# Kernel tuning notes

Hardware: AMD Instinct MI355X
Metric: run time of the kernel (lower is better)

The kernel has to match this reference:

```python
import jax, jax.numpy as jnp
import numpy as np

LN_EPS = 1e-5  # torch LayerNorm default
EPS = 1e-8     # slot-attention eps

def _ln(x, g, b):
    m = jnp.mean(x, axis=-1, keepdims=True)
    v = jnp.mean(jnp.square(x - m), axis=-1, keepdims=True)
    return (x - m) * jax.lax.rsqrt(v + LN_EPS) * g + b

def setup_inputs() -> dict:
    key = jax.random.key(0)
    ks = jax.random.split(key, 16)
    b, d, n_s, h = 131072, 256, 16, 256
    w_scale = d ** -0.5
    return {
        "inputs": jax.random.normal(ks[0], (b, 1, d), jnp.float32),
        "noise": jax.random.normal(ks[1], (n_s, d), jnp.float32),
        "slots_mu": jax.random.normal(ks[2], (1, d), jnp.float32),
        "slots_sigma": jax.random.uniform(ks[3], (1, d), jnp.float32),
        "Wq": jax.random.normal(ks[4], (d, d), jnp.float32) * w_scale,
        "bq": jnp.zeros((d,), jnp.float32),
        "Wk": jax.random.normal(ks[5], (d, d), jnp.float32) * w_scale,
        "bk": jnp.zeros((d,), jnp.float32),
        "Wv": jax.random.normal(ks[6], (d, d), jnp.float32) * w_scale,
        "bv": jnp.zeros((d,), jnp.float32),
        "W_ih": jax.random.normal(ks[7], (3 * d, d), jnp.float32) * w_scale,
        "W_hh": jax.random.normal(ks[8], (3 * d, d), jnp.float32) * w_scale,
        "b_ih": jnp.zeros((3 * d,), jnp.float32),
        "b_hh": jnp.zeros((3 * d,), jnp.float32),
        "W1": jax.random.normal(ks[9], (h, d), jnp.float32) * w_scale,
        "b1": jnp.zeros((h,), jnp.float32),
        "W2": jax.random.normal(ks[10], (d, h), jnp.float32) * (h ** -0.5),
        "b2": jnp.zeros((d,), jnp.float32),
        "g_in": jnp.ones((d,), jnp.float32),
        "be_in": jnp.zeros((d,), jnp.float32),
        "g_s": jnp.ones((d,), jnp.float32),
        "be_s": jnp.zeros((d,), jnp.float32),
        "g_f": jnp.ones((d,), jnp.float32),
        "be_f": jnp.zeros((d,), jnp.float32),
    }

def reference(inputs, noise, slots_mu, slots_sigma, Wq, bq, Wk, bk, Wv, bv,
              W_ih, W_hh, b_ih, b_hh, W1, b1, W2, b2,
              g_in, be_in, g_s, be_s, g_f, be_f):
    b, w, d = inputs.shape  # w == 1 required by the module's LayerNorm(dim)
    x = inputs.reshape(b, w * d)
    scale = d ** -0.5
    iters = 3

    slots = slots_mu + slots_sigma * noise  # (n_s, d), reparameterized normal

    x = _ln(x, g_in, be_in)
    k = x @ Wk.T + bk  # (b, d)
    v = x @ Wv.T + bv  # (b, d)

    for _ in range(iters):
        slots_prev = slots
        s = _ln(slots, g_s, be_s)
        q = s @ Wq.T + bq                      # (n_s, d)
        dots = jnp.einsum('nd,bd->nb', q, k) * scale
        attn = jax.nn.softmax(dots, axis=0) + EPS   # softmax over slots
        attn = attn / jnp.sum(attn, axis=-1, keepdims=True)
        updates = jnp.einsum('bd,nb->nd', v, attn)  # (n_s, d)
        # torch GRUCell
        gx = updates @ W_ih.T + b_ih                # (n_s, 3d)
        gh = slots_prev @ W_hh.T + b_hh
        xr, xz, xn = jnp.split(gx, 3, axis=-1)
        hr, hz, hn = jnp.split(gh, 3, axis=-1)
        r = jax.nn.sigmoid(xr + hr)
        z = jax.nn.sigmoid(xz + hz)
        n = jnp.tanh(xn + r * hn)
        slots = (1.0 - z) * n + z * slots_prev
        ff = jax.nn.relu(_ln(slots, g_f, be_f) @ W1.T + b1) @ W2.T + b2
        slots = slots + ff
    return slots
```

## Files before the change

### kernel.cpp

```cpp
#include <hip/hip_runtime.h>
#include <stdint.h>

#define B_ROWS 131072
#define SCALE 0.0625f
#define LN_EPS 1e-5f
#define ATTN_EPS 1e-8f

#define BIG_BLOCKS 512
#define BIG_THREADS 512
#define ROWS_PER_BLOCK (B_ROWS / BIG_BLOCKS)
#define ROWS_PER_WAVE  (ROWS_PER_BLOCK / 8)
#define NSLICE BIG_BLOCKS

#define WS_PARTU 0
#define WS_PARTS (WS_PARTU + NSLICE*4096)
#define WS_U     (WS_PARTS + NSLICE*16)
#define WS_S     (WS_U + 4096)
#define WS_SLOTS (WS_S + 64)
#define WS_MID   (WS_SLOTS + 4096)
#define WS_GX    (WS_MID + 4096)
#define WS_GH    (WS_GX + 12288)
#define WS_H1    (WS_GH + 12288)
#define WS_QKG   (WS_H1 + 4096)
#define WS_QB    (WS_QKG + 4096)
#define WS_WIHV  (WS_QB + 64)
#define WS_BGX   (WS_WIHV + 196608)
#define WS_WQKG  (WS_BGX + 768)
#define WS_U2G   (WS_WQKG + 65536)
#define WS_U1    (WS_U2G + 256)
#define WS_C1    (WS_U1 + 256)

__global__ __launch_bounds__(256) void k_pre1(
    const float* __restrict__ Wq, const float* __restrict__ bq,
    const float* __restrict__ Wk, const float* __restrict__ bk,
    const float* __restrict__ Wv, const float* __restrict__ bv,
    const float* __restrict__ W_ih, const float* __restrict__ b_ih,
    const float* __restrict__ g_in, const float* __restrict__ be_in,
    float* __restrict__ ws)
{
  int bid = blockIdx.x, t = threadIdx.x;
  int wave = t >> 6, lane = t & 63;
  if (bid < 192) {
    __shared__ __align__(16) float sW[4 * 256];
    __shared__ __align__(16) float sBv[256];
    int j0 = bid * 4;
#pragma unroll
    for (int r = 0; r < 4; r++) sW[r * 256 + t] = W_ih[(j0 + r) * 256 + t];
    sBv[t] = bv[t];
    __syncthreads();
    int d = t;
    float a0 = 0.f, a1 = 0.f, a2 = 0.f, a3 = 0.f;
#pragma unroll 8
    for (int dd = 0; dd < 256; dd++) {
      float v = Wv[dd * 256 + d];
      a0 = fmaf(sW[0 * 256 + dd], v, a0);
      a1 = fmaf(sW[1 * 256 + dd], v, a1);
      a2 = fmaf(sW[2 * 256 + dd], v, a2);
      a3 = fmaf(sW[3 * 256 + dd], v, a3);
    }
    ws[WS_WIHV + (j0 + 0) * 256 + d] = a0;
    ws[WS_WIHV + (j0 + 1) * 256 + d] = a1;
    ws[WS_WIHV + (j0 + 2) * 256 + d] = a2;
    ws[WS_WIHV + (j0 + 3) * 256 + d] = a3;
    float s = 0.f;
#pragma unroll
    for (int q = 0; q < 4; q++) {
      int idx = lane * 4 + q;
      s = fmaf(sW[wave * 256 + idx], sBv[idx], s);
    }
#pragma unroll
    for (int m = 1; m <= 32; m <<= 1) s += __shfl_xor(s, m);
    if (lane == 0) ws[WS_BGX + j0 + wave] = b_ih[j0 + wave] + s;
  } else if (bid < 256) {
    __shared__ __align__(16) float sKc[4 * 256];
    __shared__ __align__(16) float sBq[256];
    int c0 = (bid - 192) * 4;
#pragma unroll
    for (int r = 0; r < 4; r++) sKc[r * 256 + t] = Wk[t * 256 + c0 + r];
    sBq[t] = bq[t];
    __syncthreads();
    int d = t;
    float a0 = 0.f, a1 = 0.f, a2 = 0.f, a3 = 0.f;
#pragma unroll 8
    for (int i = 0; i < 256; i++) {
      float wq = Wq[i * 256 + d];
      a0 = fmaf(wq, sKc[0 * 256 + i], a0);
      a1 = fmaf(wq, sKc[1 * 256 + i], a1);
      a2 = fmaf(wq, sKc[2 * 256 + i], a2);
      a3 = fmaf(wq, sKc[3 * 256 + i], a3);
    }
    ws[WS_WQKG + (c0 + 0) * 256 + d] = SCALE * g_in[c0 + 0] * a0;
    ws[WS_WQKG + (c0 + 1) * 256 + d] = SCALE * g_in[c0 + 1] * a1;
    ws[WS_WQKG + (c0 + 2) * 256 + d] = SCALE * g_in[c0 + 2] * a2;
    ws[WS_WQKG + (c0 + 3) * 256 + d] = SCALE * g_in[c0 + 3] * a3;
    float s = 0.f;
#pragma unroll
    for (int q = 0; q < 4; q++) {
      int idx = lane * 4 + q;
      s = fmaf(sBq[idx], sKc[wave * 256 + idx], s);
    }
#pragma unroll
    for (int m = 1; m <= 32; m <<= 1) s += __shfl_xor(s, m);
    if (lane == 0) ws[WS_U2G + c0 + wave] = SCALE * g_in[c0 + wave] * s;
  } else {
    __shared__ __align__(16) float sBe[256];
    __shared__ __align__(16) float sT2[256];
    sBe[t] = be_in[t];
    __syncthreads();
    float a = 0.f;
#pragma unroll 8
    for (int dp = 0; dp < 256; dp += 4) {
      float4 w = *(const float4*)(Wk + t * 256 + dp);
      a = fmaf(w.x, sBe[dp], fmaf(w.y, sBe[dp + 1],
          fmaf(w.z, sBe[dp + 2], fmaf(w.w, sBe[dp + 3], a))));
    }
    sT2[t] = a + bk[t];
    __syncthreads();
    float u = 0.f;
#pragma unroll 8
    for (int i = 0; i < 256; i++)
      u = fmaf(Wq[i * 256 + t], sT2[i], u);
    ws[WS_U1 + t] = u;
    if (wave == 0) {
      float s = 0.f;
// ... 52 lines not shown
    int cr = t >> 6, n = (t >> 2) & 15, ks = t & 3;
    int c = bid * 4 + cr;
    const float* wrow = ws + WS_WQKG + c * 256 + ks * 64;
    const float* srow = &sS[n * 260 + ks * 64];
    float acc = 0.f;
#pragma unroll
    for (int i = 0; i < 16; i++) {
      float4 w = *(const float4*)(wrow + i * 4);
      float4 s4 = *(const float4*)(srow + i * 4);
      acc = fmaf(w.x, s4.x, fmaf(w.y, s4.y, fmaf(w.z, s4.z, fmaf(w.w, s4.w, acc))));
    }
    sAux[t] = acc;
    __syncthreads();
    if (t < 64) {
      int cr2 = t >> 4, n2 = t & 15;
      int c2 = bid * 4 + cr2;
      int b = cr2 * 64 + n2 * 4;
      float s = sAux[b] + sAux[b + 1] + sAux[b + 2] + sAux[b + 3];
      ws[WS_QKG + n2 * 256 + c2] = s + ws[WS_U2G + c2];
    }
  } else {
    int n = t >> 4, ks = t & 15;
    float acc = 0.f;
    for (int k = 0; k < 16; k++)
      acc = fmaf(sS[n * 260 + ks * 16 + k], ws[WS_U1 + ks * 16 + k], acc);
    sAux[t] = acc;
    __syncthreads();
    if (t < 16) {
      float s = 0.f;
      for (int k = 0; k < 16; k++) s += sAux[t * 16 + k];
      ws[WS_QB + t] = SCALE * (s + ws[WS_C1]);
    }
  }
}

__global__ __launch_bounds__(512, 2) void k_big(
    const float* __restrict__ X, float* __restrict__ ws)
{
  __shared__ __align__(16) float red[4 * 4096];
  __shared__ __align__(16) float redS[128];
  int t = threadIdx.x;
  int wave = t >> 6, lane = t & 63;
  int p = lane >> 4, g = lane & 15;

  const float* qkg = ws + WS_QKG;
  float qw[4][16];
  float qs[4];
#pragma unroll
  for (int i = 0; i < 4; i++) {
    const float* rp = qkg + (4 * p + i) * 256 + g * 16;
#pragma unroll
    for (int jq = 0; jq < 4; jq++) {
      float4 v4 = *(const float4*)(rp + 4 * jq);
      qw[i][4 * jq + 0] = v4.x; qw[i][4 * jq + 1] = v4.y;
      qw[i][4 * jq + 2] = v4.z; qw[i][4 * jq + 3] = v4.w;
    }
    float s = 0.f;
#pragma unroll
    for (int j = 0; j < 16; j++) s += qw[i][j];
    qs[i] = s;
  }
#pragma unroll
  for (int m = 1; m <= 8; m <<= 1) {
#pragma unroll
    for (int i = 0; i < 4; i++) qs[i] += __shfl_xor(qs[i], m);
  }
  float qb0[4];
  {
    float4 q4 = *(const float4*)(ws + WS_QB + 4 * p);
    qb0[0] = q4.x; qb0[1] = q4.y; qb0[2] = q4.z; qb0[3] = q4.w;
  }

  float P[4][16];
#pragma unroll
  for (int i = 0; i < 4; i++)
#pragma unroll
    for (int j = 0; j < 16; j++) P[i][j] = 0.f;
  float Q[4] = {0.f, 0.f, 0.f, 0.f};
  float Sa[4] = {0.f, 0.f, 0.f, 0.f};

  size_t rowbase = (size_t)blockIdx.x * ROWS_PER_BLOCK + (size_t)wave * ROWS_PER_WAVE;
  const float* base = X + rowbase * 256 + g * 16;

  float4 cA0 = *(const float4*)(base + 0);
  float4 cB0 = *(const float4*)(base + 4);
  float4 cC0 = *(const float4*)(base + 8);
  float4 cD0 = *(const float4*)(base + 12);
  float4 cA1 = *(const float4*)(base + 256);
  float4 cB1 = *(const float4*)(base + 260);
  float4 cC1 = *(const float4*)(base + 264);
  float4 cD1 = *(const float4*)(base + 268);

#pragma unroll 1
  for (int r = 0; r < ROWS_PER_WAVE; r += 2) {
    const float* nx = base + (size_t)((r + 2 < ROWS_PER_WAVE) ? (r + 2) : 0) * 256;
    float4 pA0 = *(const float4*)(nx + 0);
    float4 pB0 = *(const float4*)(nx + 4);
    float4 pC0 = *(const float4*)(nx + 8);
    float4 pD0 = *(const float4*)(nx + 12);
    float4 pA1 = *(const float4*)(nx + 256);
    float4 pB1 = *(const float4*)(nx + 260);
    float4 pC1 = *(const float4*)(nx + 264);
    float4 pD1 = *(const float4*)(nx + 268);

    float x0[16], x1[16];
    x0[0] = cA0.x; x0[1] = cA0.y; x0[2] = cA0.z; x0[3] = cA0.w;
    x0[4] = cB0.x; x0[5] = cB0.y; x0[6] = cB0.z; x0[7] = cB0.w;
    x0[8] = cC0.x; x0[9] = cC0.y; x0[10] = cC0.z; x0[11] = cC0.w;
    x0[12] = cD0.x; x0[13] = cD0.y; x0[14] = cD0.z; x0[15] = cD0.w;
    x1[0] = cA1.x; x1[1] = cA1.y; x1[2] = cA1.z; x1[3] = cA1.w;
    x1[4] = cB1.x; x1[5] = cB1.y; x1[6] = cB1.z; x1[7] = cB1.w;
    x1[8] = cC1.x; x1[9] = cC1.y; x1[10] = cC1.z; x1[11] = cC1.w;
    x1[12] = cD1.x; x1[13] = cD1.y; x1[14] = cD1.z; x1[15] = cD1.w;

    float s10 = 0.f, s20 = 0.f, s11 = 0.f, s21 = 0.f;
#pragma unroll
    for (int j = 0; j < 16; j++) {
      s10 += x0[j]; s20 = fmaf(x0[j], x0[j], s20);
      s11 += x1[j]; s21 = fmaf(x1[j], x1[j], s21);
    }
#pragma unroll
    for (int m = 1; m <= 8; m <<= 1) {
      s10 += __shfl_xor(s10, m); s11 += __shfl_xor(s11, m);
      s20 += __shfl_xor(s20, m); s21 += __shfl_xor(s21, m);
    }
    float mean0 = s10 * (1.f / 256.f), mean1 = s11 * (1.f / 256.f);
    float var0 = fmaxf(fmaf(-mean0, mean0, s20 * (1.f / 256.f)), 0.f);
    float var1 = fmaxf(fmaf(-mean1, mean1, s21 * (1.f / 256.f)), 0.f);
    float rs0 = rsqrtf(var0 + LN_EPS), rs1 = rsqrtf(var1 + LN_EPS);
    float mrs0 = mean0 * rs0, mrs1 = mean1 * rs1;

    float d0[4] = {0.f, 0.f, 0.f, 0.f};
    float d1[4] = {0.f, 0.f, 0.f, 0.f};
#pragma unroll
    for (int j = 0; j < 16; j++) {
#pragma unroll
      for (int i = 0; i < 4; i++) {
        d0[i] = fmaf(qw[i][j], x0[j], d0[i]);
        d1[i] = fmaf(qw[i][j], x1[j], d1[i]);
      }
    }
#pragma unroll
    for (int m = 1; m <= 8; m <<= 1) {
#pragma unroll
      for (int i = 0; i < 4; i++) {
        d0[i] += __shfl_xor(d0[i], m);
        d1[i] += __shfl_xor(d1[i], m);
      }
    }
    float dsc0[4], dsc1[4];
#pragma unroll
    for (int i = 0; i < 4; i++) {
      dsc0[i] = fmaf(rs0, d0[i], fmaf(-mrs0, qs[i], qb0[i]));
      dsc1[i] = fmaf(rs1, d1[i], fmaf(-mrs1, qs[i], qb0[i]));
    }

    float mx0 = fmaxf(fmaxf(dsc0[0], dsc0[1]), fmaxf(dsc0[2], dsc0[3]));
    float mx1 = fmaxf(fmaxf(dsc1[0], dsc1[1]), fmaxf(dsc1[2], dsc1[3]));
    mx0 = fmaxf(mx0, __shfl_xor(mx0, 16)); mx1 = fmaxf(mx1, __shfl_xor(mx1, 16));
    mx0 = fmaxf(mx0, __shfl_xor(mx0, 32)); mx1 = fmaxf(mx1, __shfl_xor(mx1, 32));
    float e0[4], e1[4];
#pragma unroll
    for (int i = 0; i < 4; i++) {
      e0[i] = __expf(dsc0[i] - mx0);
      e1[i] = __expf(dsc1[i] - mx1);
    }
    float se0 = e0[0] + e0[1] + e0[2] + e0[3];
    float se1 = e1[0] + e1[1] + e1[2] + e1[3];
    se0 += __shfl_xor(se0, 16); se1 += __shfl_xor(se1, 16);
    se0 += __shfl_xor(se0, 32); se1 += __shfl_xor(se1, 32);
    float inv0 = 1.0f / se0, inv1 = 1.0f / se1;
    float a0v[4], ar0[4], a1v[4], ar1[4];
#pragma unroll
    for (int i = 0; i < 4; i++) {
      a0v[i] = fmaf(e0[i], inv0, ATTN_EPS); ar0[i] = a0v[i] * rs0;
      a1v[i] = fmaf(e1[i], inv1, ATTN_EPS); ar1[i] = a1v[i] * rs1;
    }

#pragma unroll
    for (int j = 0; j < 16; j++) {
#pragma unroll
      for (int i = 0; i < 4; i++) {
        P[i][j] = fmaf(ar0[i], x0[j], P[i][j]);
        P[i][j] = fmaf(ar1[i], x1[j], P[i][j]);
      }
    }
#pragma unroll
    for (int i = 0; i < 4; i++) {
      Q[i] = fmaf(a0v[i], mrs0, Q[i]);
      Q[i] = fmaf(a1v[i], mrs1, Q[i]);
      Sa[i] += a0v[i];
      Sa[i] += a1v[i];
    }

    cA0 = pA0; cB0 = pB0; cC0 = pC0; cD0 = pD0;
    cA1 = pA1; cB1 = pB1; cC1 = pC1; cD1 = pD1;
  }

  int slot = wave & 3;
  if (wave < 4) {
#pragma unroll
    for (int i = 0; i < 4; i++) {
#pragma unroll
      for (int jq = 0; jq < 4; jq++) {
        float4 v4;
        v4.x = P[i][4 * jq + 0] - Q[i]; v4.y = P[i][4 * jq + 1] - Q[i];
        v4.z = P[i][4 * jq + 2] - Q[i]; v4.w = P[i][4 * jq + 3] - Q[i];
        *(float4*)&red[slot * 4096 + (4 * p + i) * 256 + g * 16 + jq * 4] = v4;
      }
    }
  }
  if (g == 0) {
#pragma unroll
    for (int i = 0; i < 4; i++) redS[wave * 16 + 4 * p + i] = Sa[i];
  }
  __syncthreads();
  if (wave >= 4) {
#pragma unroll
    for (int i = 0; i < 4; i++) {
#pragma unroll
      for (int jq = 0; jq < 4; jq++) {
        float4* dst = (float4*)&red[slot * 4096 + (4 * p + i) * 256 + g * 16 + jq * 4];
        float4 c = *dst;
        c.x += P[i][4 * jq + 0] - Q[i]; c.y += P[i][4 * jq + 1] - Q[i];
        c.z += P[i][4 * jq + 2] - Q[i]; c.w += P[i][4 * jq + 3] - Q[i];
        *dst = c;
      }
    }
  }
  __syncthreads();
#pragma unroll
  for (int k = 0; k < 8; k++) {
    int idx = k * 512 + t;
    float v = red[idx] + red[4096 + idx] + red[8192 + idx] + red[12288 + idx];
    ws[WS_PARTU + (size_t)blockIdx.x * 4096 + idx] = v;
  }
  if (t < 16) {
    float sv = 0.f;
#pragma unroll
    for (int w = 0; w < 8; w++) sv += redS[w * 16 + t];
    ws[WS_PARTS + blockIdx.x * 16 + t] = sv;
  }
}

__global__ __launch_bounds__(256) void k_red(float* __restrict__ ws)
{
  __shared__ __align__(16) float sAux[256];
  int bid = blockIdx.x, t = threadIdx.x;
  if (bid < 256) {
    int el = t & 15, wg = t >> 4;
    int e = bid * 16 + el;
    float acc = 0.f;
#pragma unroll 8
    for (int k = 0; k < 32; k++)
      acc += ws[WS_PARTU + (size_t)(wg + k * 16) * 4096 + e];
    sAux[t] = acc;
    __syncthreads();
    if (t < 16) {
      float s = 0.f;
      for (int w = 0; w < 16; w++) s += sAux[w * 16 + t];
      ws[WS_U + bid * 16 + t] = s;
    }
  } else {
    int n = t & 15, wg = t >> 4;
    float acc = 0.f;
#pragma unroll 8
    for (int k = 0; k < 32; k++)
      acc += ws[WS_PARTS + (wg + k * 16) * 16 + n];
    sAux[t] = acc;
    __syncthreads();
    if (t < 16) {
      float s = 0.f;
      for (int w = 0; w < 16; w++) s += sAux[w * 16 + t];
      ws[WS_S + t] = s;
    }
  }
}

__global__ __launch_bounds__(256) void k_gxgh(
    const float* __restrict__ W_hh, const float* __restrict__ b_hh,
    const float* __restrict__ g_in, const float* __restrict__ be_in,
    float* __restrict__ ws)
{
  __shared__ __align__(16) float sU[16 * 260];
  __shared__ __align__(16) float sInv[16];
  int bid = blockIdx.x, t = threadIdx.x;
  bool isgx = bid < 64;
  if (isgx && t < 16) sInv[t] = 1.0f / ws[WS_S + t];
  __syncthreads();
  if (isgx) {
    float gi = g_in[t], bi = be_in[t];
    for (int n = 0; n < 16; n++)
      sU[n * 260 + t] = fmaf(gi * ws[WS_U + n * 256 + t], sInv[n], bi);
  } else {
    for (int n = 0; n < 16; n++)
      sU[n * 260 + t] = ws[WS_SLOTS + n * 256 + t];
  }
  __syncthreads();
  int jr = t >> 4, n = t & 15;
  if (jr < 12) {
    int j = (isgx ? bid : bid - 64) * 12 + jr;
    const float* srow = &sU[n * 260];
    const float* wrow = isgx ? (ws + WS_WIHV + j * 256) : (W_hh + j * 256);
    float acc = isgx ? ws[WS_BGX + j] : b_hh[j];
#pragma unroll 8
    for (int k = 0; k < 64; k++) {
      float4 w = *(const float4*)(wrow + k * 4);
      float4 s4 = *(const float4*)(srow + k * 4);
      acc = fmaf(w.x, s4.x, fmaf(w.y, s4.y, fmaf(w.z, s4.z, fmaf(w.w, s4.w, acc))));
    }
    if (isgx) ws[WS_GX + n * 768 + j] = acc;
    else      ws[WS_GH + n * 768 + j] = acc;
  }
}

__global__ __launch_bounds__(256) void k_midh1(
    const float* __restrict__ W1, const float* __restrict__ b1,
    const float* __restrict__ g_f, const float* __restrict__ be_f,
    float* __restrict__ ws)
{
  __shared__ __align__(16) float sM[16 * 260];
  __shared__ __align__(16) float sAux[512];
  __shared__ __align__(16) float sStat[32];
  int bid = blockIdx.x, t = threadIdx.x;
  for (int n = 0; n < 16; n++) {
    float xr = ws[WS_GX + n * 768 + t],       hr = ws[WS_GH + n * 768 + t];
    float xz = ws[WS_GX + n * 768 + 256 + t], hz = ws[WS_GH + n * 768 + 256 + t];
    float xn = ws[WS_GX + n * 768 + 512 + t], hn = ws[WS_GH + n * 768 + 512 + t];
    float sp = ws[WS_SLOTS + n * 256 + t];
    float r = 1.f / (1.f + __expf(-(xr + hr)));
    float z = 1.f / (1.f + __expf(-(xz + hz)));
    float nn = tanhf(fmaf(r, hn, xn));
    float mid = fmaf(z, sp - nn, nn);
    sM[n * 260 + t] = mid;
    if (bid == 0) ws[WS_MID + n * 256 + t] = mid;
  }
  __syncthreads();
  { int n = t >> 4, c = t & 15;
    float s1 = 0.f, s2 = 0.f;
    for (int k = 0; k < 16; k++) {
      float x = sM[n * 260 + c * 16 + k];
      s1 += x; s2 = fmaf(x, x, s2);
    }
    sAux[n * 16 + c] = s1; sAux[256 + n * 16 + c] = s2; }
  __syncthreads();
  if (t < 16) {
    float s1 = 0.f, s2 = 0.f;
    for (int c = 0; c < 16; c++) { s1 += sAux[t * 16 + c]; s2 += sAux[256 + t * 16 + c]; }
    float m = s1 * (1.f / 256.f);
    float v = fmaxf(fmaf(-m, m, s2 * (1.f / 256.f)), 0.f);
    sStat[t] = m; sStat[16 + t] = rsqrtf(v + LN_EPS);
  }
  __syncthreads();
  { float gf = g_f[t], bf = be_f[t];
    for (int n = 0; n < 16; n++) {
      float m = sStat[n], rs = sStat[16 + n];
      sM[n * 260 + t] = fmaf((sM[n * 260 + t] - m) * rs, gf, bf);
    } }
  __syncthreads();
  int jr = t >> 6, n = (t >> 2) & 15, ks = t & 3;
  int j = bid * 4 + jr;
  const float* wrow = W1 + j * 256 + ks * 64;
  const float* srow = &sM[n * 260 + ks * 64];
  float acc = 0.f;
#pragma unroll
  for (int k = 0; k < 16; k++) {
    float4 w = *(const float4*)(wrow + k * 4);
    float4 s4 = *(const float4*)(srow + k * 4);
    acc = fmaf(w.x, s4.x, fmaf(w.y, s4.y, fmaf(w.z, s4.z, fmaf(w.w, s4.w, acc))));
  }
  sAux[t] = acc;
  __syncthreads();
  if (t < 64) {
    int jr2 = t >> 4, n2 = t & 15;
    int j2 = bid * 4 + jr2;
    int b = jr2 * 64 + n2 * 4;
    float s = sAux[b] + sAux[b + 1] + sAux[b + 2] + sAux[b + 3] + b1[j2];
    ws[WS_H1 + n2 * 256 + j2] = fmaxf(s, 0.f);
  }
}

__global__ __launch_bounds__(256) void k_ffnew(
    const float* __restrict__ W2, const float* __restrict__ b2v,
    float* __restrict__ out, float* __restrict__ ws)
{
  __shared__ __align__(16) float sH[16 * 260];
  __shared__ __align__(16) float sAux[256];
  int bid = blockIdx.x, t = threadIdx.x;
  for (int n = 0; n < 16; n++)
    sH[n * 260 + t] = ws[WS_H1 + n * 256 + t];
  __syncthreads();
  int dr = t >> 6, n = (t >> 2) & 15, ks = t & 3;
  int d = bid * 4 + dr;
  const float* wrow = W2 + d * 256 + ks * 64;
  const float* srow = &sH[n * 260 + ks * 64];
  float acc = 0.f;
#pragma unroll
  for (int k = 0; k < 16; k++) {
    float4 w = *(const float4*)(wrow + k * 4);
    float4 s4 = *(const float4*)(srow + k * 4);
    acc = fmaf(w.x, s4.x, fmaf(w.y, s4.y, fmaf(w.z, s4.z, fmaf(w.w, s4.w, acc))));
  }
  sAux[t] = acc;
  __syncthreads();
  if (t < 64) {
    int dr2 = t >> 4, n2 = t & 15;
    int d2 = bid * 4 + dr2;
    int b = dr2 * 64 + n2 * 4;
    float s = sAux[b] + sAux[b + 1] + sAux[b + 2] + sAux[b + 3]
            + b2v[d2] + ws[WS_MID + n2 * 256 + d2];
    ws[WS_SLOTS + n2 * 256 + d2] = s;
    out[n2 * 256 + d2] = s;
  }
}

extern "C" void kernel_launch(void* const* d_in, const int* in_sizes, int n_in,
                              void* d_out, int out_size, void* d_ws, size_t ws_size,
                              hipStream_t stream)
{
  (void)in_sizes; (void)n_in; (void)out_size; (void)ws_size;
  const float* inputs = (const float*)d_in[0];
  const float* noise  = (const float*)d_in[1];
  const float* mu     = (const float*)d_in[2];
  const float* sigma  = (const float*)d_in[3];
  const float* Wq     = (const float*)d_in[4];
  const float* bq     = (const float*)d_in[5];
  const float* Wk     = (const float*)d_in[6];
  const float* bk     = (const float*)d_in[7];
  const float* Wv     = (const float*)d_in[8];
  const float* bv     = (const float*)d_in[9];
  const float* W_ih   = (const float*)d_in[10];
  const float* W_hh   = (const float*)d_in[11];
  const float* b_ih   = (const float*)d_in[12];
  const float* b_hh   = (const float*)d_in[13];
  const float* W1     = (const float*)d_in[14];
  const float* b1     = (const float*)d_in[15];
  const float* W2     = (const float*)d_in[16];
  const float* b2     = (const float*)d_in[17];
  const float* g_in   = (const float*)d_in[18];
  const float* be_in  = (const float*)d_in[19];
  const float* g_s    = (const float*)d_in[20];
  const float* be_s   = (const float*)d_in[21];
  const float* g_f    = (const float*)d_in[22];
  const float* be_f   = (const float*)d_in[23];
  float* ws = (float*)d_ws;
  float* out = (float*)d_out;

  hipLaunchKernelGGL(k_pre1, dim3(257), dim3(256), 0, stream,
                     Wq, bq, Wk, bk, Wv, bv, W_ih, b_ih, g_in, be_in, ws);
  hipLaunchKernelGGL(k_qkg, dim3(65), dim3(256), 0, stream,
                     noise, mu, sigma, g_s, be_s, ws, 1);
  for (int it = 0; it < 3; it++) {
    hipLaunchKernelGGL(k_big, dim3(BIG_BLOCKS), dim3(BIG_THREADS), 0, stream, inputs, ws);
    hipLaunchKernelGGL(k_red, dim3(257), dim3(256), 0, stream, ws);
    hipLaunchKernelGGL(k_gxgh, dim3(128), dim3(256), 0, stream,
                       W_hh, b_hh, g_in, be_in, ws);
    hipLaunchKernelGGL(k_midh1, dim3(64), dim3(256), 0, stream,
                       W1, b1, g_f, be_f, ws);
    hipLaunchKernelGGL(k_ffnew, dim3(64), dim3(256), 0, stream,
                       W2, b2, out, ws);
    if (it < 2)
      hipLaunchKernelGGL(k_qkg, dim3(65), dim3(256), 0, stream,
                         noise, mu, sigma, g_s, be_s, ws, 0);
  }
}
```

Before: 551.0 us.

## Fuse per-iteration slot update chain into one per-slot kernel

Replaces the reduction, GRU gate GEMVs, LayerNorm+MLP and next-iteration query prep kernels with a single kernel that runs one 512-thread block per slot. Each block reduces the partial updates for its slot, computes the GRU, feed-forward and next query/key projection with wave-shuffle dot products, and writes the new slots. This removes four launches and their global round trips per iteration. In exchange only 16 blocks run, and each block rereads all the weight matrices, so the grid is very narrow and leans on cache bandwidth.

```diff
diff --git a/kernel.cpp b/kernel.cpp
--- a/kernel.cpp
+++ b/kernel.cpp
@@ -30,6 +30,28 @@
 #define WS_U1    (WS_U2G + 256)
 #define WS_C1    (WS_U1 + 256)
 
+__device__ __forceinline__ float dot16(const float* __restrict__ w, const float* s)
+{
+  float4 w0 = *(const float4*)(w);
+  float4 w1 = *(const float4*)(w + 4);
+  float4 w2 = *(const float4*)(w + 8);
+  float4 w3 = *(const float4*)(w + 12);
+  float4 s0 = *(const float4*)(s);
+  float4 s1 = *(const float4*)(s + 4);
+  float4 s2 = *(const float4*)(s + 8);
+  float4 s3 = *(const float4*)(s + 12);
+  float a = 0.f;
+  a = fmaf(w0.x, s0.x, a); a = fmaf(w0.y, s0.y, a);
+  a = fmaf(w0.z, s0.z, a); a = fmaf(w0.w, s0.w, a);
+  a = fmaf(w1.x, s1.x, a); a = fmaf(w1.y, s1.y, a);
+  a = fmaf(w1.z, s1.z, a); a = fmaf(w1.w, s1.w, a);
+  a = fmaf(w2.x, s2.x, a); a = fmaf(w2.y, s2.y, a);
+  a = fmaf(w2.z, s2.z, a); a = fmaf(w2.w, s2.w, a);
+  a = fmaf(w3.x, s3.x, a); a = fmaf(w3.y, s3.y, a);
+  a = fmaf(w3.z, s3.z, a); a = fmaf(w3.w, s3.w, a);
+  return a;
+}
+
 __global__ __launch_bounds__(256) void k_pre1(
     const float* __restrict__ Wq, const float* __restrict__ bq,
     const float* __restrict__ Wk, const float* __restrict__ bk,
@@ -419,174 +441,166 @@
   }
 }
 
-__global__ __launch_bounds__(256) void k_red(float* __restrict__ ws)
-{
-  __shared__ __align__(16) float sAux[256];
-  int bid = blockIdx.x, t = threadIdx.x;
-  if (bid < 256) {
-    int el = t & 15, wg = t >> 4;
-    int e = bid * 16 + el;
-    float acc = 0.f;
-#pragma unroll 8
-    for (int k = 0; k < 32; k++)
-      acc += ws[WS_PARTU + (size_t)(wg + k * 16) * 4096 + e];
-    sAux[t] = acc;
-    __syncthreads();
-    if (t < 16) {
-      float s = 0.f;
-      for (int w = 0; w < 16; w++) s += sAux[w * 16 + t];
-      ws[WS_U + bid * 16 + t] = s;
-    }
-  } else {
-    int n = t & 15, wg = t >> 4;
-    float acc = 0.f;
-#pragma unroll 8
-    for (int k = 0; k < 32; k++)
-      acc += ws[WS_PARTS + (wg + k * 16) * 16 + n];
-    sAux[t] = acc;
-    __syncthreads();
-    if (t < 16) {
-      float s = 0.f;
-      for (int w = 0; w < 16; w++) s += sAux[w * 16 + t];
-      ws[WS_S + t] = s;
-    }
-  }
-}
-
-__global__ __launch_bounds__(256) void k_gxgh(
+__global__ __launch_bounds__(512) void k_slot2(
     const float* __restrict__ W_hh, const float* __restrict__ b_hh,
     const float* __restrict__ g_in, const float* __restrict__ be_in,
-    float* __restrict__ ws)
-{
-  __shared__ __align__(16) float sU[16 * 260];
-  __shared__ __align__(16) float sInv[16];
-  int bid = blockIdx.x, t = threadIdx.x;
-  bool isgx = bid < 64;
-  if (isgx && t < 16) sInv[t] = 1.0f / ws[WS_S + t];
-  __syncthreads();
-  if (isgx) {
-    float gi = g_in[t], bi = be_in[t];
-    for (int n = 0; n < 16; n++)
-      sU[n * 260 + t] = fmaf(gi * ws[WS_U + n * 256 + t], sInv[n], bi);
-  } else {
-    for (int n = 0; n < 16; n++)
-      sU[n * 260 + t] = ws[WS_SLOTS + n * 256 + t];
-  }
-  __syncthreads();
-  int jr = t >> 4, n = t & 15;
-  if (jr < 12) {
-    int j = (isgx ? bid : bid - 64) * 12 + jr;
-    const float* srow = &sU[n * 260];
-    const float* wrow = isgx ? (ws + WS_WIHV + j * 256) : (W_hh + j * 256);
-    float acc = isgx ? ws[WS_BGX + j] : b_hh[j];
-#pragma unroll 8
-    for (int k = 0; k < 64; k++) {
-      float4 w = *(const float4*)(wrow + k * 4);
-      float4 s4 = *(const float4*)(srow + k * 4);
-      acc = fmaf(w.x, s4.x, fmaf(w.y, s4.y, fmaf(w.z, s4.z, fmaf(w.w, s4.w, acc))));
-    }
-    if (isgx) ws[WS_GX + n * 768 + j] = acc;
-    else      ws[WS_GH + n * 768 + j] = acc;
-  }
-}
-
-__global__ __launch_bounds__(256) void k_midh1(
     const float* __restrict__ W1, const float* __restrict__ b1,
     const float* __restrict__ g_f, const float* __restrict__ be_f,
-    float* __restrict__ ws)
+    const float* __restrict__ W2, const float* __restrict__ b2v,
+    const float* __restrict__ g_s, const float* __restrict__ be_s,
+    float* __restrict__ out, float* __restrict__ ws, int last)
 {
-  __shared__ __align__(16) float sM[16 * 260];
-  __shared__ __align__(16) float sAux[512];
-  __shared__ __align__(16) float sStat[32];
-  int bid = blockIdx.x, t = threadIdx.x;
-  for (int n = 0; n < 16; n++) {
-    float xr = ws[WS_GX + n * 768 + t],       hr = ws[WS_GH + n * 768 + t];
-    float xz = ws[WS_GX + n * 768 + 256 + t], hz = ws[WS_GH + n * 768 + 256 + t];
-    float xn = ws[WS_GX + n * 768 + 512 + t], hn = ws[WS_GH + n * 768 + 512 + t];
-    float sp = ws[WS_SLOTS + n * 256 + t];
+  __shared__ __align__(16) float sUpd[256];
+  __shared__ __align__(16) float sSp[256];
+  __shared__ __align__(16) float sGX[768];
+  __shared__ __align__(16) float sGH[768];
+  __shared__ __align__(16) float sMid[256];
+  __shared__ __align__(16) float sVec[256];
+  __shared__ __align__(16) float sH1[256];
+  __shared__ __align__(16) float sNew[256];
+  __shared__ __align__(16) float sR[16];
+  __shared__ __align__(16) float sT[512];
+  int n = blockIdx.x, t = threadIdx.x;
+  int wv = t >> 6, lane = t & 63;
+  int j4 = t >> 4, kt = t & 15;
+  int tt = t & 255, th = t >> 8;
+
+  {
+    float u = 0.f;
+    const float* pu = ws + WS_PARTU + (size_t)th * 256 * 4096 + n * 256 + tt;
+#pragma unroll 16
+    for (int s = 0; s < 256; s++) u += pu[(size_t)s * 4096];
+    sT[t] = u;
+    float sa = ws[WS_PARTS + t * 16 + n];
+#pragma unroll
+    for (int m = 1; m <= 32; m <<= 1) sa += __shfl_xor(sa, m);
+    if (lane == 0) sR[wv] = sa;
+  }
+  __syncthreads();
+  {
+    float S = sR[0] + sR[1] + sR[2] + sR[3] + sR[4] + sR[5] + sR[6] + sR[7];
+    float invS = 1.0f / S;
+    if (t < 256) {
+      float uu = sT[t] + sT[256 + t];
+      sUpd[t] = fmaf(g_in[t] * uu, invS, be_in[t]);
+      sSp[t] = ws[WS_SLOTS + n * 256 + t];
+    }
+  }
+  __syncthreads();
+
+#pragma unroll 2
+  for (int pass = 0; pass < 24; pass++) {
+    int j = pass * 32 + j4;
+    float a = dot16(ws + WS_WIHV + (size_t)j * 256 + kt * 16, sUpd + kt * 16);
+    a += __shfl_xor(a, 1); a += __shfl_xor(a, 2);
+    a += __shfl_xor(a, 4); a += __shfl_xor(a, 8);
+    if (kt == 0) sGX[j] = a + ws[WS_BGX + j];
+  }
+#pragma unroll 2
+  for (int pass = 0; pass < 24; pass++) {
+    int j = pass * 32 + j4;
+    float a = dot16(W_hh + (size_t)j * 256 + kt * 16, sSp + kt * 16);
+    a += __shfl_xor(a, 1); a += __shfl_xor(a, 2);
+    a += __shfl_xor(a, 4); a += __shfl_xor(a, 8);
+    if (kt == 0) sGH[j] = a + b_hh[j];
+  }
+  __syncthreads();
+
+  float mid = 0.f;
+  if (t < 256) {
+    float xr = sGX[t], xz = sGX[256 + t], xn = sGX[512 + t];
+    float hr = sGH[t], hz = sGH[256 + t], hn = sGH[512 + t];
+    float sp = sSp[t];
     float r = 1.f / (1.f + __expf(-(xr + hr)));
     float z = 1.f / (1.f + __expf(-(xz + hz)));
     float nn = tanhf(fmaf(r, hn, xn));
-    float mid = fmaf(z, sp - nn, nn);
-    sM[n * 260 + t] = mid;
-    if (bid == 0) ws[WS_MID + n * 256 + t] = mid;
-  }
-  __syncthreads();
-  { int n = t >> 4, c = t & 15;
-    float s1 = 0.f, s2 = 0.f;
-    for (int k = 0; k < 16; k++) {
-      float x = sM[n * 260 + c * 16 + k];
-      s1 += x; s2 = fmaf(x, x, s2);
-    }
-    sAux[n * 16 + c] = s1; sAux[256 + n * 16 + c] = s2; }
-  __syncthreads();
-  if (t < 16) {
-    float s1 = 0.f, s2 = 0.f;
-    for (int c = 0; c < 16; c++) { s1 += sAux[t * 16 + c]; s2 += sAux[256 + t * 16 + c]; }
-    float m = s1 * (1.f / 256.f);
-    float v = fmaxf(fmaf(-m, m, s2 * (1.f / 256.f)), 0.f);
-    sStat[t] = m; sStat[16 + t] = rsqrtf(v + LN_EPS);
-  }
-  __syncthreads();
-  { float gf = g_f[t], bf = be_f[t];
-    for (int n = 0; n < 16; n++) {
-      float m = sStat[n], rs = sStat[16 + n];
-      sM[n * 260 + t] = fmaf((sM[n * 260 + t] - m) * rs, gf, bf);
-    } }
-  __syncthreads();
-  int jr = t >> 6, n = (t >> 2) & 15, ks = t & 3;
-  int j = bid * 4 + jr;
-  const float* wrow = W1 + j * 256 + ks * 64;
-  const float* srow = &sM[n * 260 + ks * 64];
-  float acc = 0.f;
-#pragma unroll
-  for (int k = 0; k < 16; k++) {
-    float4 w = *(const float4*)(wrow + k * 4);
-    float4 s4 = *(const float4*)(srow + k * 4);
-    acc = fmaf(w.x, s4.x, fmaf(w.y, s4.y, fmaf(w.z, s4.z, fmaf(w.w, s4.w, acc))));
-  }
-  sAux[t] = acc;
-  __syncthreads();
-  if (t < 64) {
-    int jr2 = t >> 4, n2 = t & 15;
-    int j2 = bid * 4 + jr2;
-    int b = jr2 * 64 + n2 * 4;
-    float s = sAux[b] + sAux[b + 1] + sAux[b + 2] + sAux[b + 3] + b1[j2];
-    ws[WS_H1 + n2 * 256 + j2] = fmaxf(s, 0.f);
-  }
-}
-
-__global__ __launch_bounds__(256) void k_ffnew(
-    const float* __restrict__ W2, const float* __restrict__ b2v,
-    float* __restrict__ out, float* __restrict__ ws)
-{
-  __shared__ __align__(16) float sH[16 * 260];
-  __shared__ __align__(16) float sAux[256];
-  int bid = blockIdx.x, t = threadIdx.x;
-  for (int n = 0; n < 16; n++)
-    sH[n * 260 + t] = ws[WS_H1 + n * 256 + t];
-  __syncthreads();
-  int dr = t >> 6, n = (t >> 2) & 15, ks = t & 3;
-  int d = bid * 4 + dr;
-  const float* wrow = W2 + d * 256 + ks * 64;
-  const float* srow = &sH[n * 260 + ks * 64];
-  float acc = 0.f;
-#pragma unroll
-  for (int k = 0; k < 16; k++) {
-    float4 w = *(const float4*)(wrow + k * 4);
-    float4 s4 = *(const float4*)(srow + k * 4);
-    acc = fmaf(w.x, s4.x, fmaf(w.y, s4.y, fmaf(w.z, s4.z, fmaf(w.w, s4.w, acc))));
-  }
-  sAux[t] = acc;
-  __syncthreads();
-  if (t < 64) {
-    int dr2 = t >> 4, n2 = t & 15;
-    int d2 = bid * 4 + dr2;
-    int b = dr2 * 64 + n2 * 4;
-    float s = sAux[b] + sAux[b + 1] + sAux[b + 2] + sAux[b + 3]
-            + b2v[d2] + ws[WS_MID + n2 * 256 + d2];
-    ws[WS_SLOTS + n2 * 256 + d2] = s;
-    out[n2 * 256 + d2] = s;
+    mid = fmaf(z, sp - nn, nn);
+    sMid[t] = mid;
+  }
+  {
+    float s1 = mid, s2 = mid * mid;
+#pragma unroll
+    for (int m = 1; m <= 32; m <<= 1) {
+      s1 += __shfl_xor(s1, m); s2 += __shfl_xor(s2, m);
+    }
+    if (lane == 0) { sR[wv] = s1; sR[8 + wv] = s2; }
+  }
+  __syncthreads();
+  {
+    float s1 = sR[0] + sR[1] + sR[2] + sR[3] + sR[4] + sR[5] + sR[6] + sR[7];
+    float s2 = sR[8] + sR[9] + sR[10] + sR[11] + sR[12] + sR[13] + sR[14] + sR[15];
+    float mean = s1 * (1.f / 256.f);
+    float var = fmaxf(fmaf(-mean, mean, s2 * (1.f / 256.f)), 0.f);
+    float rs = rsqrtf(var + LN_EPS);
+    if (t < 256)
+      sVec[t] = fmaf((sMid[t] - mean) * rs, g_f[t], be_f[t]);
+  }
+  __syncthreads();
+
+#pragma unroll 2
+  for (int pass = 0; pass < 8; pass++) {
+    int j = pass * 32 + j4;
+    float a = dot16(W1 + (size_t)j * 256 + kt * 16, sVec + kt * 16);
+    a += __shfl_xor(a, 1); a += __shfl_xor(a, 2);
+    a += __shfl_xor(a, 4); a += __shfl_xor(a, 8);
+    if (kt == 0) sH1[j] = fmaxf(a + b1[j], 0.f);
+  }
+  __syncthreads();
+
+#pragma unroll 2
+  for (int pass = 0; pass < 8; pass++) {
+    int d = pass * 32 + j4;
+    float a = dot16(W2 + (size_t)d * 256 + kt * 16, sH1 + kt * 16);
+    a += __shfl_xor(a, 1); a += __shfl_xor(a, 2);
+    a += __shfl_xor(a, 4); a += __shfl_xor(a, 8);
+    if (kt == 0) sNew[d] = a + b2v[d] + sMid[d];
+  }
+  __syncthreads();
+  if (t < 256) {
+    float v = sNew[t];
+    ws[WS_SLOTS + n * 256 + t] = v;
+    out[n * 256 + t] = v;
+  }
+  if (last) return;
+
+  {
+    float v = (t < 256) ? sNew[t] : 0.f;
+    float s1 = v, s2 = v * v;
+#pragma unroll
+    for (int m = 1; m <= 32; m <<= 1) {
+      s1 += __shfl_xor(s1, m); s2 += __shfl_xor(s2, m);
+    }
+    if (lane == 0) { sR[wv] = s1; sR[8 + wv] = s2; }
+  }
+  __syncthreads();
+  {
+    float s1 = sR[0] + sR[1] + sR[2] + sR[3] + sR[4] + sR[5] + sR[6] + sR[7];
+    float s2 = sR[8] + sR[9] + sR[10] + sR[11] + sR[12] + sR[13] + sR[14] + sR[15];
+    float mean = s1 * (1.f / 256.f);
+    float var = fmaxf(fmaf(-mean, mean, s2 * (1.f / 256.f)), 0.f);
+    float rs = rsqrtf(var + LN_EPS);
+    if (t < 256)
+      sVec[t] = fmaf((sNew[t] - mean) * rs, g_s[t], be_s[t]);
+  }
+  __syncthreads();
+#pragma unroll 2
+  for (int pass = 0; pass < 8; pass++) {
+    int c = pass * 32 + j4;
+    float a = dot16(ws + WS_WQKG + (size_t)c * 256 + kt * 16, sVec + kt * 16);
+    a += __shfl_xor(a, 1); a += __shfl_xor(a, 2);
+    a += __shfl_xor(a, 4); a += __shfl_xor(a, 8);
+    if (kt == 0) ws[WS_QKG + n * 256 + c] = a + ws[WS_U2G + c];
+  }
+  {
+    float pq = (t < 256) ? sVec[t] * ws[WS_U1 + t] : 0.f;
+#pragma unroll
+    for (int m = 1; m <= 32; m <<= 1) pq += __shfl_xor(pq, m);
+    if (lane == 0) sR[wv] = pq;
+  }
+  __syncthreads();
+  if (t == 0) {
+    float s = sR[0] + sR[1] + sR[2] + sR[3] + sR[4] + sR[5] + sR[6] + sR[7];
+    ws[WS_QB + n] = SCALE * (s + ws[WS_C1]);
   }
 }
 
@@ -628,15 +642,8 @@
                      noise, mu, sigma, g_s, be_s, ws, 1);
   for (int it = 0; it < 3; it++) {
     hipLaunchKernelGGL(k_big, dim3(BIG_BLOCKS), dim3(BIG_THREADS), 0, stream, inputs, ws);
-    hipLaunchKernelGGL(k_red, dim3(257), dim3(256), 0, stream, ws);
-    hipLaunchKernelGGL(k_gxgh, dim3(128), dim3(256), 0, stream,
-                       W_hh, b_hh, g_in, be_in, ws);
-    hipLaunchKernelGGL(k_midh1, dim3(64), dim3(256), 0, stream,
-                       W1, b1, g_f, be_f, ws);
-    hipLaunchKernelGGL(k_ffnew, dim3(64), dim3(256), 0, stream,
-                       W2, b2, out, ws);
-    if (it < 2)
-      hipLaunchKernelGGL(k_qkg, dim3(65), dim3(256), 0, stream,
-                         noise, mu, sigma, g_s, be_s, ws, 0);
+    hipLaunchKernelGGL(k_slot2, dim3(16), dim3(512), 0, stream,
+                       W_hh, b_hh, g_in, be_in, W1, b1, g_f, be_f,
+                       W2, b2, g_s, be_s, out, ws, (it == 2) ? 1 : 0);
   }
 }
```

After: 665.5 us. +20.8%, slower.

## Accumulate block partials into 64 atomic slices and process four rows per iteration

Applied to the files above, without the earlier changes.

Each big block now atomically adds its partial slot updates and attention sums into one of 64 slices instead of writing its own 512-way partial. The reduction kernel reads only 64 slices and zeroes them for the next iteration, and the pre-kernel zeroes them initially. This cuts reduction traffic. The main loop also handles four rows at a time without explicit software prefetch, which raises ILP but also register pressure. Atomics add contention and make summation order nondeterministic.

```diff
diff --git a/kernel.cpp b/kernel.cpp
--- a/kernel.cpp
+++ b/kernel.cpp
@@ -10,11 +10,11 @@
 #define BIG_THREADS 512
 #define ROWS_PER_BLOCK (B_ROWS / BIG_BLOCKS)
 #define ROWS_PER_WAVE  (ROWS_PER_BLOCK / 8)
-#define NSLICE BIG_BLOCKS
+#define NSLICE 64
 
 #define WS_PARTU 0
-#define WS_PARTS (WS_PARTU + NSLICE*4096)
-#define WS_U     (WS_PARTS + NSLICE*16)
+#define WS_PARTS (WS_PARTU + 512*4096)
+#define WS_U     (WS_PARTS + 512*16)
 #define WS_S     (WS_U + 4096)
 #define WS_SLOTS (WS_S + 64)
 #define WS_MID   (WS_SLOTS + 4096)
@@ -40,6 +40,15 @@
 {
   int bid = blockIdx.x, t = threadIdx.x;
   int wave = t >> 6, lane = t & 63;
+  if (bid < 256) {
+#pragma unroll
+    for (int q = 0; q < 4; q++)
+      ws[WS_PARTU + bid * 1024 + q * 256 + t] = 0.f;
+  } else {
+#pragma unroll
+    for (int q = 0; q < 4; q++)
+      ws[WS_PARTS + q * 256 + t] = 0.f;
+  }
   if (bid < 192) {
     __shared__ __align__(16) float sW[4 * 256];
     __shared__ __align__(16) float sBv[256];
@@ -258,119 +267,114 @@
   size_t rowbase = (size_t)blockIdx.x * ROWS_PER_BLOCK + (size_t)wave * ROWS_PER_WAVE;
   const float* base = X + rowbase * 256 + g * 16;
 
-  float4 cA0 = *(const float4*)(base + 0);
-  float4 cB0 = *(const float4*)(base + 4);
-  float4 cC0 = *(const float4*)(base + 8);
-  float4 cD0 = *(const float4*)(base + 12);
-  float4 cA1 = *(const float4*)(base + 256);
-  float4 cB1 = *(const float4*)(base + 260);
-  float4 cC1 = *(const float4*)(base + 264);
-  float4 cD1 = *(const float4*)(base + 268);
-
 #pragma unroll 1
-  for (int r = 0; r < ROWS_PER_WAVE; r += 2) {
-    const float* nx = base + (size_t)((r + 2 < ROWS_PER_WAVE) ? (r + 2) : 0) * 256;
-    float4 pA0 = *(const float4*)(nx + 0);
-    float4 pB0 = *(const float4*)(nx + 4);
-    float4 pC0 = *(const float4*)(nx + 8);
-    float4 pD0 = *(const float4*)(nx + 12);
-    float4 pA1 = *(const float4*)(nx + 256);
-    float4 pB1 = *(const float4*)(nx + 260);
-    float4 pC1 = *(const float4*)(nx + 264);
-    float4 pD1 = *(const float4*)(nx + 268);
-
-    float x0[16], x1[16];
-    x0[0] = cA0.x; x0[1] = cA0.y; x0[2] = cA0.z; x0[3] = cA0.w;
-    x0[4] = cB0.x; x0[5] = cB0.y; x0[6] = cB0.z; x0[7] = cB0.w;
-    x0[8] = cC0.x; x0[9] = cC0.y; x0[10] = cC0.z; x0[11] = cC0.w;
-    x0[12] = cD0.x; x0[13] = cD0.y; x0[14] = cD0.z; x0[15] = cD0.w;
-    x1[0] = cA1.x; x1[1] = cA1.y; x1[2] = cA1.z; x1[3] = cA1.w;
-    x1[4] = cB1.x; x1[5] = cB1.y; x1[6] = cB1.z; x1[7] = cB1.w;
-    x1[8] = cC1.x; x1[9] = cC1.y; x1[10] = cC1.z; x1[11] = cC1.w;
-    x1[12] = cD1.x; x1[13] = cD1.y; x1[14] = cD1.z; x1[15] = cD1.w;
-
-    float s10 = 0.f, s20 = 0.f, s11 = 0.f, s21 = 0.f;
+  for (int r = 0; r < ROWS_PER_WAVE; r += 4) {
+    const float* rp = base + (size_t)r * 256;
+    float x[4][16];
+#pragma unroll
+    for (int i = 0; i < 4; i++) {
+      float4 a = *(const float4*)(rp + i * 256 + 0);
+      float4 b = *(const float4*)(rp + i * 256 + 4);
+      float4 c = *(const float4*)(rp + i * 256 + 8);
+      float4 d = *(const float4*)(rp + i * 256 + 12);
+      x[i][0] = a.x; x[i][1] = a.y; x[i][2] = a.z; x[i][3] = a.w;
+      x[i][4] = b.x; x[i][5] = b.y; x[i][6] = b.z; x[i][7] = b.w;
+      x[i][8] = c.x; x[i][9] = c.y; x[i][10] = c.z; x[i][11] = c.w;
+      x[i][12] = d.x; x[i][13] = d.y; x[i][14] = d.z; x[i][15] = d.w;
+    }
+
+    float s1[4] = {0.f, 0.f, 0.f, 0.f};
+    float s2[4] = {0.f, 0.f, 0.f, 0.f};
 #pragma unroll
     for (int j = 0; j < 16; j++) {
-      s10 += x0[j]; s20 = fmaf(x0[j], x0[j], s20);
-      s11 += x1[j]; s21 = fmaf(x1[j], x1[j], s21);
+#pragma unroll
+      for (int i = 0; i < 4; i++) {
+        s1[i] += x[i][j];
+        s2[i] = fmaf(x[i][j], x[i][j], s2[i]);
+      }
     }
 #pragma unroll
     for (int m = 1; m <= 8; m <<= 1) {
-      s10 += __shfl_xor(s10, m); s11 += __shfl_xor(s11, m);
-      s20 += __shfl_xor(s20, m); s21 += __shfl_xor(s21, m);
-    }
-    float mean0 = s10 * (1.f / 256.f), mean1 = s11 * (1.f / 256.f);
-    float var0 = fmaxf(fmaf(-mean0, mean0, s20 * (1.f / 256.f)), 0.f);
-    float var1 = fmaxf(fmaf(-mean1, mean1, s21 * (1.f / 256.f)), 0.f);
-    float rs0 = rsqrtf(var0 + LN_EPS), rs1 = rsqrtf(var1 + LN_EPS);
-    float mrs0 = mean0 * rs0, mrs1 = mean1 * rs1;
-
-    float d0[4] = {0.f, 0.f, 0.f, 0.f};
-    float d1[4] = {0.f, 0.f, 0.f, 0.f};
+#pragma unroll
+      for (int i = 0; i < 4; i++) {
+        s1[i] += __shfl_xor(s1[i], m);
+        s2[i] += __shfl_xor(s2[i], m);
+      }
+    }
+    float rs[4], mrs[4];
+#pragma unroll
+    for (int i = 0; i < 4; i++) {
+      float mean = s1[i] * (1.f / 256.f);
+      float var = fmaxf(fmaf(-mean, mean, s2[i] * (1.f / 256.f)), 0.f);
+      rs[i] = rsqrtf(var + LN_EPS);
+      mrs[i] = mean * rs[i];
+    }
+
+    float dd[4][4];
+#pragma unroll
+    for (int i = 0; i < 4; i++)
+#pragma unroll
+      for (int sl = 0; sl < 4; sl++) dd[i][sl] = 0.f;
 #pragma unroll
     for (int j = 0; j < 16; j++) {
 #pragma unroll
       for (int i = 0; i < 4; i++) {
-        d0[i] = fmaf(qw[i][j], x0[j], d0[i]);
-        d1[i] = fmaf(qw[i][j], x1[j], d1[i]);
+#pragma unroll
+        for (int sl = 0; sl < 4; sl++)
+          dd[i][sl] = fmaf(qw[sl][j], x[i][j], dd[i][sl]);
       }
     }
 #pragma unroll
     for (int m = 1; m <= 8; m <<= 1) {
 #pragma unroll
       for (int i = 0; i < 4; i++) {
-        d0[i] += __shfl_xor(d0[i], m);
-        d1[i] += __shfl_xor(d1[i], m);
-      }
-    }
-    float dsc0[4], dsc1[4];
+#pragma unroll
+        for (int sl = 0; sl < 4; sl++)
+          dd[i][sl] += __shfl_xor(dd[i][sl], m);
+      }
+    }
+
+    float ar[4][4], av[4][4];
 #pragma unroll
     for (int i = 0; i < 4; i++) {
-      dsc0[i] = fmaf(rs0, d0[i], fmaf(-mrs0, qs[i], qb0[i]));
-      dsc1[i] = fmaf(rs1, d1[i], fmaf(-mrs1, qs[i], qb0[i]));
-    }
-
-    float mx0 = fmaxf(fmaxf(dsc0[0], dsc0[1]), fmaxf(dsc0[2], dsc0[3]));
-    float mx1 = fmaxf(fmaxf(dsc1[0], dsc1[1]), fmaxf(dsc1[2], dsc1[3]));
-    mx0 = fmaxf(mx0, __shfl_xor(mx0, 16)); mx1 = fmaxf(mx1, __shfl_xor(mx1, 16));
-    mx0 = fmaxf(mx0, __shfl_xor(mx0, 32)); mx1 = fmaxf(mx1, __shfl_xor(mx1, 32));
-    float e0[4], e1[4];
+      float dsc[4];
+#pragma unroll
+      for (int sl = 0; sl < 4; sl++)
+        dsc[sl] = fmaf(rs[i], dd[i][sl], fmaf(-mrs[i], qs[sl], qb0[sl]));
+      float mx = fmaxf(fmaxf(dsc[0], dsc[1]), fmaxf(dsc[2], dsc[3]));
+      mx = fmaxf(mx, __shfl_xor(mx, 16));
+      mx = fmaxf(mx, __shfl_xor(mx, 32));
+      float e[4];
+#pragma unroll
+      for (int sl = 0; sl < 4; sl++) e[sl] = __expf(dsc[sl] - mx);
+      float se = e[0] + e[1] + e[2] + e[3];
+      se += __shfl_xor(se, 16);
+      se += __shfl_xor(se, 32);
+      float inv = 1.0f / se;
+#pragma unroll
+      for (int sl = 0; sl < 4; sl++) {
+        av[i][sl] = fmaf(e[sl], inv, ATTN_EPS);
+        ar[i][sl] = av[i][sl] * rs[i];
+      }
+    }
+
+#pragma unroll
+    for (int j = 0; j < 16; j++) {
+#pragma unroll
+      for (int i = 0; i < 4; i++) {
+#pragma unroll
+        for (int sl = 0; sl < 4; sl++)
+          P[sl][j] = fmaf(ar[i][sl], x[i][j], P[sl][j]);
+      }
+    }
 #pragma unroll
     for (int i = 0; i < 4; i++) {
-      e0[i] = __expf(dsc0[i] - mx0);
-      e1[i] = __expf(dsc1[i] - mx1);
-    }
-    float se0 = e0[0] + e0[1] + e0[2] + e0[3];
-    float se1 = e1[0] + e1[1] + e1[2] + e1[3];
-    se0 += __shfl_xor(se0, 16); se1 += __shfl_xor(se1, 16);
-    se0 += __shfl_xor(se0, 32); se1 += __shfl_xor(se1, 32);
-    float inv0 = 1.0f / se0, inv1 = 1.0f / se1;
-    float a0v[4], ar0[4], a1v[4], ar1[4];
-#pragma unroll
-    for (int i = 0; i < 4; i++) {
-      a0v[i] = fmaf(e0[i], inv0, ATTN_EPS); ar0[i] = a0v[i] * rs0;
-      a1v[i] = fmaf(e1[i], inv1, ATTN_EPS); ar1[i] = a1v[i] * rs1;
-    }
-
-#pragma unroll
-    for (int j = 0; j < 16; j++) {
-#pragma unroll
-      for (int i = 0; i < 4; i++) {
-        P[i][j] = fmaf(ar0[i], x0[j], P[i][j]);
-        P[i][j] = fmaf(ar1[i], x1[j], P[i][j]);
-      }
-    }
-#pragma unroll
-    for (int i = 0; i < 4; i++) {
-      Q[i] = fmaf(a0v[i], mrs0, Q[i]);
-      Q[i] = fmaf(a1v[i], mrs1, Q[i]);
-      Sa[i] += a0v[i];
-      Sa[i] += a1v[i];
-    }
-
-    cA0 = pA0; cB0 = pB0; cC0 = pC0; cD0 = pD0;
-    cA1 = pA1; cB1 = pB1; cC1 = pC1; cD1 = pD1;
+#pragma unroll
+      for (int sl = 0; sl < 4; sl++) {
+        Q[sl] = fmaf(av[i][sl], mrs[i], Q[sl]);
+        Sa[sl] += av[i][sl];
+      }
+    }
   }
 
   int slot = wave & 3;
@@ -405,17 +409,18 @@
     }
   }
   __syncthreads();
+  int slice = blockIdx.x & 63;
 #pragma unroll
   for (int k = 0; k < 8; k++) {
     int idx = k * 512 + t;
     float v = red[idx] + red[4096 + idx] + red[8192 + idx] + red[12288 + idx];
-    ws[WS_PARTU + (size_t)blockIdx.x * 4096 + idx] = v;
+    atomicAdd(&ws[WS_PARTU + (size_t)slice * 4096 + idx], v);
   }
   if (t < 16) {
     float sv = 0.f;
 #pragma unroll
     for (int w = 0; w < 8; w++) sv += redS[w * 16 + t];
-    ws[WS_PARTS + blockIdx.x * 16 + t] = sv;
+    atomicAdd(&ws[WS_PARTS + slice * 16 + t], sv);
   }
 }
 
@@ -427,9 +432,12 @@
     int el = t & 15, wg = t >> 4;
     int e = bid * 16 + el;
     float acc = 0.f;
-#pragma unroll 8
-    for (int k = 0; k < 32; k++)
-      acc += ws[WS_PARTU + (size_t)(wg + k * 16) * 4096 + e];
+#pragma unroll
+    for (int k = 0; k < 4; k++) {
+      size_t idx = WS_PARTU + (size_t)(wg + k * 16) * 4096 + e;
+      acc += ws[idx];
+      ws[idx] = 0.f;
+    }
     sAux[t] = acc;
     __syncthreads();
     if (t < 16) {
@@ -440,9 +448,12 @@
   } else {
     int n = t & 15, wg = t >> 4;
     float acc = 0.f;
-#pragma unroll 8
-    for (int k = 0; k < 32; k++)
-      acc += ws[WS_PARTS + (wg + k * 16) * 16 + n];
+#pragma unroll
+    for (int k = 0; k < 4; k++) {
+      int idx = WS_PARTS + (wg + k * 16) * 16 + n;
+      acc += ws[idx];
+      ws[idx] = 0.f;
+    }
     sAux[t] = acc;
     __syncthreads();
     if (t < 16) {
```

After: 674.2 us. 1.22x slower.

## Reduce attention partials into 64 atomic slices and fuse LN stats with dot products

Applied to the files above, without the earlier changes.

Each of the 512 big blocks now atomically adds its partial updates and sums into one of 64 slices instead of writing its own slice. This shrinks the workspace the reduction kernel must read by a factor of eight. The reduction kernel zeroes the slices after reading them, and the pre-kernel zeroes them at startup, so they are reusable across iterations. The LayerNorm statistics loop is also merged with the q·x dot-product loop and its shuffles. The cost is atomic contention (8 blocks per slice) and nondeterministic float summation order.

```diff
diff --git a/kernel.cpp b/kernel.cpp
--- a/kernel.cpp
+++ b/kernel.cpp
@@ -10,11 +10,11 @@
 #define BIG_THREADS 512
 #define ROWS_PER_BLOCK (B_ROWS / BIG_BLOCKS)
 #define ROWS_PER_WAVE  (ROWS_PER_BLOCK / 8)
-#define NSLICE BIG_BLOCKS
+#define NSLICE 64
 
 #define WS_PARTU 0
-#define WS_PARTS (WS_PARTU + NSLICE*4096)
-#define WS_U     (WS_PARTS + NSLICE*16)
+#define WS_PARTS (WS_PARTU + 512*4096)
+#define WS_U     (WS_PARTS + 512*16)
 #define WS_S     (WS_U + 4096)
 #define WS_SLOTS (WS_S + 64)
 #define WS_MID   (WS_SLOTS + 4096)
@@ -40,6 +40,15 @@
 {
   int bid = blockIdx.x, t = threadIdx.x;
   int wave = t >> 6, lane = t & 63;
+  if (bid < 256) {
+#pragma unroll
+    for (int q = 0; q < 4; q++)
+      ws[WS_PARTU + bid * 1024 + q * 256 + t] = 0.f;
+  } else {
+#pragma unroll
+    for (int q = 0; q < 4; q++)
+      ws[WS_PARTS + q * 256 + t] = 0.f;
+  }
   if (bid < 192) {
     __shared__ __align__(16) float sW[4 * 256];
     __shared__ __align__(16) float sBv[256];
@@ -290,15 +299,27 @@
     x1[12] = cD1.x; x1[13] = cD1.y; x1[14] = cD1.z; x1[15] = cD1.w;
 
     float s10 = 0.f, s20 = 0.f, s11 = 0.f, s21 = 0.f;
+    float d0[4] = {0.f, 0.f, 0.f, 0.f};
+    float d1[4] = {0.f, 0.f, 0.f, 0.f};
 #pragma unroll
     for (int j = 0; j < 16; j++) {
       s10 += x0[j]; s20 = fmaf(x0[j], x0[j], s20);
       s11 += x1[j]; s21 = fmaf(x1[j], x1[j], s21);
+#pragma unroll
+      for (int i = 0; i < 4; i++) {
+        d0[i] = fmaf(qw[i][j], x0[j], d0[i]);
+        d1[i] = fmaf(qw[i][j], x1[j], d1[i]);
+      }
     }
 #pragma unroll
     for (int m = 1; m <= 8; m <<= 1) {
       s10 += __shfl_xor(s10, m); s11 += __shfl_xor(s11, m);
       s20 += __shfl_xor(s20, m); s21 += __shfl_xor(s21, m);
+#pragma unroll
+      for (int i = 0; i < 4; i++) {
+        d0[i] += __shfl_xor(d0[i], m);
+        d1[i] += __shfl_xor(d1[i], m);
+      }
     }
     float mean0 = s10 * (1.f / 256.f), mean1 = s11 * (1.f / 256.f);
     float var0 = fmaxf(fmaf(-mean0, mean0, s20 * (1.f / 256.f)), 0.f);
@@ -306,24 +327,6 @@
     float rs0 = rsqrtf(var0 + LN_EPS), rs1 = rsqrtf(var1 + LN_EPS);
     float mrs0 = mean0 * rs0, mrs1 = mean1 * rs1;
 
-    float d0[4] = {0.f, 0.f, 0.f, 0.f};
-    float d1[4] = {0.f, 0.f, 0.f, 0.f};
-#pragma unroll
-    for (int j = 0; j < 16; j++) {
-#pragma unroll
-      for (int i = 0; i < 4; i++) {
-        d0[i] = fmaf(qw[i][j], x0[j], d0[i]);
-        d1[i] = fmaf(qw[i][j], x1[j], d1[i]);
-      }
-    }
-#pragma unroll
-    for (int m = 1; m <= 8; m <<= 1) {
-#pragma unroll
-      for (int i = 0; i < 4; i++) {
-        d0[i] += __shfl_xor(d0[i], m);
-        d1[i] += __shfl_xor(d1[i], m);
-      }
-    }
     float dsc0[4], dsc1[4];
 #pragma unroll
     for (int i = 0; i < 4; i++) {
@@ -405,17 +408,18 @@
     }
   }
   __syncthreads();
+  int slice = blockIdx.x & 63;
 #pragma unroll
   for (int k = 0; k < 8; k++) {
     int idx = k * 512 + t;
     float v = red[idx] + red[4096 + idx] + red[8192 + idx] + red[12288 + idx];
-    ws[WS_PARTU + (size_t)blockIdx.x * 4096 + idx] = v;
+    atomicAdd(&ws[WS_PARTU + (size_t)slice * 4096 + idx], v);
   }
   if (t < 16) {
     float sv = 0.f;
 #pragma unroll
     for (int w = 0; w < 8; w++) sv += redS[w * 16 + t];
-    ws[WS_PARTS + blockIdx.x * 16 + t] = sv;
+    atomicAdd(&ws[WS_PARTS + slice * 16 + t], sv);
   }
 }
 
@@ -427,9 +431,12 @@
     int el = t & 15, wg = t >> 4;
     int e = bid * 16 + el;
     float acc = 0.f;
-#pragma unroll 8
-    for (int k = 0; k < 32; k++)
-      acc += ws[WS_PARTU + (size_t)(wg + k * 16) * 4096 + e];
+#pragma unroll
+    for (int k = 0; k < 4; k++) {
+      size_t idx = WS_PARTU + (size_t)(wg + k * 16) * 4096 + e;
+      acc += ws[idx];
+      ws[idx] = 0.f;
+    }
     sAux[t] = acc;
     __syncthreads();
     if (t < 16) {
@@ -440,9 +447,12 @@
   } else {
     int n = t & 15, wg = t >> 4;
     float acc = 0.f;
-#pragma unroll 8
-    for (int k = 0; k < 32; k++)
-      acc += ws[WS_PARTS + (wg + k * 16) * 16 + n];
+#pragma unroll
+    for (int k = 0; k < 4; k++) {
+      int idx = WS_PARTS + (wg + k * 16) * 16 + n;
+      acc += ws[idx];
+      ws[idx] = 0.f;
+    }
     sAux[t] = acc;
     __syncthreads();
     if (t < 16) {
```

Measured after the change: 557.5 us. No clear change (+1.2%).
